# Performance work log

Hardware: AMD Instinct MI355X
Metric: run time of the kernel (lower is better)

Reference implementation:

```python
import jax, jax.numpy as jnp
import numpy as np

TEMP = 5.0      # torch_kmeans SoftKMeans default temperature
N_ITERS = 25    # fixed iteration count (tolerance-based stop removed for jit)
EPS = 1e-9


def _soft_kmeans(x, l, key):
    # x: (r, q, d) -> labels (r, q) int32, centers (r, l, d)
    r, q, d = x.shape
    keys = jax.random.split(key, r)
    # random-point init (one permutation per batch, first l points)
    idx = jax.vmap(lambda k: jax.random.permutation(k, q)[:l])(keys)  # (r, l)
    centers = jnp.take_along_axis(x, idx[:, :, None], axis=1)         # (r, l, d)
    x_sq = jnp.sum(x * x, axis=-1)                                    # (r, q)

    def dist_to(centers):
        # squared euclidean distance (r, q, l)
        return (x_sq[:, :, None]
                - 2.0 * jnp.einsum('rqd,rld->rql', x, centers)
                + jnp.sum(centers * centers, axis=-1)[:, None, :])

    def step(centers, _):
        w = jax.nn.softmax(-TEMP * dist_to(centers), axis=-1)         # (r, q, l)
        denom = jnp.sum(w, axis=1)[:, :, None] + EPS                  # (r, l, 1)
        centers = jnp.einsum('rql,rqd->rld', w, x) / denom
        return centers, None

    centers, _ = jax.lax.scan(step, centers, None, length=N_ITERS)
    labels = jnp.argmin(dist_to(centers), axis=-1)                    # (r, q)
    return labels, centers


def setup_inputs() -> dict:
    key = jax.random.key(0)
    x = jax.random.normal(key, (8, 2048, 1024), dtype=jnp.float32)
    return {"x": x, "q": 4096, "r": 8, "l": 256}


def reference(x, q, r, l):
    B, T, F = x.shape
    # B*T*F must equal r*q*d; mirrors x.view(B,-1).view(B,q,-1).view(r,q,-1)
    xr = x.reshape(r, q, -1)
    labels, centers = _soft_kmeans(xr, l, jax.random.key(42))
    # gather centroid per point: rec[b, i, :] = centers[b, labels[b, i], :]
    rec = jnp.take_along_axis(centers, labels[:, :, None], axis=1)    # (r, q, d)
    return rec.reshape(B, T, F)
```

## Files before the change

kernel.cpp:

```cpp
#include <hip/hip_runtime.h>
#include <stdint.h>

#define RB 8
#define QN 4096
#define DN 512
#define LN 256
#define NITERS 25

typedef double f64x4 __attribute__((ext_vector_type(4)));

__device__ __forceinline__ void tf2x32(uint32_t k0, uint32_t k1,
                                       uint32_t x0, uint32_t x1,
                                       uint32_t& y0, uint32_t& y1) {
  uint32_t ks2 = k0 ^ k1 ^ 0x1BD11BDAu;
#define TFR(r) { x0 += x1; x1 = (x1 << (r)) | (x1 >> (32 - (r))); x1 ^= x0; }
  x0 += k0; x1 += k1;
  TFR(13) TFR(15) TFR(26) TFR(6)   x0 += k1;  x1 += ks2 + 1u;
  TFR(17) TFR(29) TFR(16) TFR(24)  x0 += ks2; x1 += k0 + 2u;
  TFR(13) TFR(15) TFR(26) TFR(6)   x0 += k0;  x1 += k1 + 3u;
  TFR(17) TFR(29) TFR(16) TFR(24)  x0 += k1;  x1 += ks2 + 4u;
  TFR(13) TFR(15) TFR(26) TFR(6)   x0 += ks2; x1 += k0 + 5u;
#undef TFR
  y0 = x0; y1 = x1;
}

__global__ __launch_bounds__(1024) void k_init(const float* __restrict__ x,
                                               float* __restrict__ centers) {
  __shared__ unsigned long long comp[QN];
  __shared__ unsigned short perm[QN];
  __shared__ unsigned short ptmp[QN];
  const int b = blockIdx.x, t = threadIdx.x;

  uint32_t kb0, kb1;
  tf2x32(0u, 42u, 0u, (uint32_t)b, kb0, kb1);

  for (int i = t; i < QN; i += 1024) perm[i] = (unsigned short)i;
  __syncthreads();

  for (int round = 0; round < 2; ++round) {
    uint32_t nk0, nk1, sk0, sk1;
    tf2x32(kb0, kb1, 0u, 0u, nk0, nk1);
    tf2x32(kb0, kb1, 0u, 1u, sk0, sk1);
    kb0 = nk0; kb1 = nk1;
    for (int i = t; i < QN; i += 1024) {
      uint32_t y0, y1;
      tf2x32(sk0, sk1, 0u, (uint32_t)i, y0, y1);
      uint32_t bits = y0 ^ y1;
      comp[i] = ((unsigned long long)bits << 32) | (unsigned)i;
    }
    __syncthreads();
    for (int k = 2; k <= QN; k <<= 1) {
      for (int j = k >> 1; j > 0; j >>= 1) {
        for (int i = t; i < QN; i += 1024) {
          int ixj = i ^ j;
          if (ixj > i) {
            unsigned long long vi = comp[i], vj = comp[ixj];
            bool up = ((i & k) == 0);
            bool sw = up ? (vi > vj) : (vi < vj);
            if (sw) { comp[i] = vj; comp[ixj] = vi; }
          }
        }
        __syncthreads();
      }
    }
    for (int i = t; i < QN; i += 1024) ptmp[i] = perm[(unsigned)(comp[i] & 0xFFFFu)];
    __syncthreads();
    for (int i = t; i < QN; i += 1024) perm[i] = ptmp[i];
    __syncthreads();
  }

  const float4* xb = (const float4*)(x + (size_t)b * QN * DN);
  float4* cb = (float4*)(centers + (size_t)b * LN * DN);
  for (int e = t; e < LN * (DN / 4); e += 1024) {
    int row = e >> 7;
    int c = e & 127;
    cb[(size_t)row * 128 + c] = xb[(size_t)perm[row] * 128 + c];
  }
}

__global__ __launch_bounds__(256) void k_rowsq_d(const float* __restrict__ a,
                                                 double* __restrict__ o, int nrows) {
  int w = (blockIdx.x * 256 + threadIdx.x) >> 6;
  int lane = threadIdx.x & 63;
  if (w >= nrows) return;
  const float* row = a + (size_t)w * DN;
  double s = 0.0;
  for (int i = lane; i < DN; i += 64) { double v = (double)row[i]; s = fma(v, v, s); }
#pragma unroll
  for (int off = 32; off; off >>= 1) s += __shfl_down(s, off);
  if (lane == 0) o[w] = s;
}

__global__ __launch_bounds__(64) void k_probe(int* __restrict__ flag) {
  __shared__ double xT[16][17];
  __shared__ double cT[16][17];
  const int t = threadIdx.x;
  for (int i = t; i < 256; i += 64) {
    int r = i >> 4, d = i & 15;
    xT[d][r] = (double)(r * 5 + d * 3 + 1);
    cT[d][r] = (double)(r * 2 + d * 7 + 2);
  }
  __syncthreads();
  const int kg = t >> 4, li = t & 15;
  f64x4 acc = {0.0, 0.0, 0.0, 0.0};
#pragma unroll
  for (int kk = 0; kk < 4; kk++) {
    double a  = xT[kk * 4 + kg][li];
    double bv = cT[kk * 4 + kg][li];
    acc = __builtin_amdgcn_mfma_f64_16x16x4f64(a, bv, acc, 0, 0, 0);
  }
  bool ok1 = true, ok2 = true;
#pragma unroll
  for (int d = 0; d < 4; d++) {
    int q1 = kg * 4 + d;
    int q2 = kg + 4 * d;
    double ref1 = 0.0, ref2 = 0.0;
    for (int dd = 0; dd < 16; dd++) {
      ref1 += xT[dd][q1] * cT[dd][li];
      ref2 += xT[dd][q2] * cT[dd][li];
    }
    ok1 = ok1 && (acc[d] == ref1);
    ok2 = ok2 && (acc[d] == ref2);
  }
  unsigned long long v1 = __ballot(ok1);
  unsigned long long v2 = __ballot(ok2);
  if (t == 0) *flag = (v1 == ~0ull) ? 1 : ((v2 == ~0ull) ? 2 : 0);
}

#define QT 64
#define XPD 68
#define CPD 260
#define DK 16
#define XLD 82
#define CLDf 260
__device__ __forceinline__ int grow(int q) { return q + ((q >> 3) << 1); }

#define ARENA_D 5888

__global__ __launch_bounds__(256, 2) void k_assign(const float* __restrict__ x,
                                                   const float* __restrict__ centers,
                                                   const double* __restrict__ csqd,
                                                   float* __restrict__ W,
                                                   const int* __restrict__ flag) {
  __shared__ double arena[ARENA_D];
  const int mode = *flag;
  const int b = blockIdx.y, q0 = blockIdx.x * QT, t = threadIdx.x;
  const float* xb = x + ((size_t)b * QN + q0) * DN;
  const float* cb = centers + (size_t)b * LN * DN;
  const int xrow = t >> 2, xc4 = t & 3;

  if (mode != 0) {
    double (*xT)[XPD]  = (double(*)[XPD])arena;
    double (*cT)[CPD]  = (double(*)[CPD])(arena + 16 * XPD);
    double (*redm)[5]  = (double(*)[5])(arena + 16 * XPD + 16 * CPD);
    double (*reds)[5]  = (double(*)[5])(arena + 16 * XPD + 16 * CPD + 320);
    const int w = t >> 6, lane = t & 63;
    const int kg = lane >> 4, li = lane & 15;

    f64x4 acc[4][4];
#pragma unroll
    for (int i = 0; i < 4; i++)
#pragma unroll
      for (int j = 0; j < 4; j++) acc[i][j] = (f64x4){0.0, 0.0, 0.0, 0.0};

    float4 gx, gc[4];
    gx = *(const float4*)(xb + (size_t)xrow * DN + xc4 * 4);
#pragma unroll
    for (int i = 0; i < 4; i++) {
      int f = t + 256 * i; int row = f >> 2, c4 = f & 3;
      gc[i] = *(const float4*)(cb + (size_t)row * DN + c4 * 4);
    }

    for (int d0 = 0; d0 < DN; d0 += 16) {
      xT[xc4 * 4 + 0][xrow] = (double)gx.x;
      xT[xc4 * 4 + 1][xrow] = (double)gx.y;
      xT[xc4 * 4 + 2][xrow] = (double)gx.z;
      xT[xc4 * 4 + 3][xrow] = (double)gx.w;
#pragma unroll
      for (int i = 0; i < 4; i++) {
        int f = t + 256 * i; int row = f >> 2, c4 = f & 3;
        cT[c4 * 4 + 0][row] = (double)gc[i].x;
        cT[c4 * 4 + 1][row] = (double)gc[i].y;
        cT[c4 * 4 + 2][row] = (double)gc[i].z;
        cT[c4 * 4 + 3][row] = (double)gc[i].w;
      }
      __syncthreads();
      if (d0 + 16 < DN) {
        gx = *(const float4*)(xb + (size_t)xrow * DN + (d0 + 16) + xc4 * 4);
#pragma unroll
        for (int i = 0; i < 4; i++) {
          int f = t + 256 * i; int row = f >> 2, c4 = f & 3;
          gc[i] = *(const float4*)(cb + (size_t)row * DN + (d0 + 16) + c4 * 4);
        }
      }
#pragma unroll
      for (int kk = 0; kk < 4; kk++) {
        double a[4], bf[4];
#pragma unroll
        for (int qt = 0; qt < 4; qt++) a[qt] = xT[kk * 4 + kg][qt * 16 + li];
#pragma unroll
        for (int lt = 0; lt < 4; lt++) bf[lt] = cT[kk * 4 + kg][w * 64 + lt * 16 + li];
#pragma unroll
        for (int qt = 0; qt < 4; qt++)
#pragma unroll
          for (int lt = 0; lt < 4; lt++)
            acc[qt][lt] = __builtin_amdgcn_mfma_f64_16x16x4f64(a[qt], bf[lt], acc[qt][lt], 0, 0, 0);
      }
      __syncthreads();
    }

    double csqv[4];
#pragma unroll
    for (int lt = 0; lt < 4; lt++) csqv[lt] = csqd[b * LN + w * 64 + lt * 16 + li];

    double rm[4][4];
#pragma unroll
    for (int qt = 0; qt < 4; qt++)
#pragma unroll
      for (int d = 0; d < 4; d++) {
        double m = -1e300;
#pragma unroll
        for (int lt = 0; lt < 4; lt++) {
          double lg = -5.0 * (csqv[lt] - 2.0 * acc[qt][lt][d]);
          acc[qt][lt][d] = lg;
          m = fmax(m, lg);
        }
        rm[qt][d] = m;
      }
#pragma unroll
    for (int off = 1; off < 16; off <<= 1)
#pragma unroll
      for (int qt = 0; qt < 4; qt++)
#pragma unroll
        for (int d = 0; d < 4; d++) rm[qt][d] = fmax(rm[qt][d], __shfl_xor(rm[qt][d], off, 64));
    if (li == 0) {
#pragma unroll
      for (int qt = 0; qt < 4; qt++)
#pragma unroll
        for (int d = 0; d < 4; d++) {
          int qr = qt * 16 + ((mode == 1) ? (kg * 4 + d) : (kg + 4 * d));
          redm[qr][w] = rm[qt][d];
        }
    }
    __syncthreads();
#pragma unroll
    for (int qt = 0; qt < 4; qt++)
#pragma unroll
      for (int d = 0; d < 4; d++) {
        int qr = qt * 16 + ((mode == 1) ? (kg * 4 + d) : (kg + 4 * d));
        rm[qt][d] = fmax(fmax(redm[qr][0], redm[qr][1]), fmax(redm[qr][2], redm[qr][3]));
      }
    double sv[4][4];
#pragma unroll
    for (int qt = 0; qt < 4; qt++)
#pragma unroll
      for (int d = 0; d < 4; d++) {
        double s = 0.0;
#pragma unroll
        for (int lt = 0; lt < 4; lt++) {
          double e = exp(acc[qt][lt][d] - rm[qt][d]);
          acc[qt][lt][d] = e;
          s += e;
        }
        sv[qt][d] = s;
      }
#pragma unroll
    for (int off = 1; off < 16; off <<= 1)
#pragma unroll
      for (int qt = 0; qt < 4; qt++)
#pragma unroll
        for (int d = 0; d < 4; d++) sv[qt][d] += __shfl_xor(sv[qt][d], off, 64);
    if (li == 0) {
#pragma unroll
      for (int qt = 0; qt < 4; qt++)
#pragma unroll
        for (int d = 0; d < 4; d++) {
          int qr = qt * 16 + ((mode == 1) ? (kg * 4 + d) : (kg + 4 * d));
          reds[qr][w] = sv[qt][d];
        }
    }
    __syncthreads();
#pragma unroll
    for (int qt = 0; qt < 4; qt++)
#pragma unroll
      for (int d = 0; d < 4; d++) {
        int qr = qt * 16 + ((mode == 1) ? (kg * 4 + d) : (kg + 4 * d));
        double tot = reds[qr][0] + reds[qr][1] + reds[qr][2] + reds[qr][3];
        double inv = 1.0 / tot;
        float* wr = W + ((size_t)b * QN + q0 + qr) * LN + w * 64 + li;
#pragma unroll
        for (int lt = 0; lt < 4; lt++)
          wr[lt * 16] = (float)(acc[qt][lt][d] * inv);
      }
  } else {
    double (*xsD)[XLD]  = (double(*)[XLD])arena;
    float  (*csF)[CLDf] = (float(*)[CLDf])(arena + 16 * XLD);
    double (*red)[33]   = (double(*)[33])(arena + 16 * XLD + (16 * CLDf) / 2);
    const int rg = t & 7, cg = t >> 3;
    double acc[8][8];
#pragma unroll
    for (int i = 0; i < 8; i++)
#pragma unroll
      for (int j = 0; j < 8; j++) acc[i][j] = 0.0;

    const int xg = grow(xrow);
    float4 gx, gc[4];
    gx = *(const float4*)(xb + (size_t)xrow * DN + xc4 * 4);
#pragma unroll
    for (int i = 0; i < 4; i++) {
      int f = t + 256 * i; int row = f >> 2, c4 = f & 3;
      gc[i] = *(const float4*)(cb + (size_t)row * DN + c4 * 4);
    }

    for (int d0 = 0; d0 < DN; d0 += DK) {
      xsD[xc4 * 4 + 0][xg] = (double)gx.x; xsD[xc4 * 4 + 1][xg] = (double)gx.y;
      xsD[xc4 * 4 + 2][xg] = (double)gx.z; xsD[xc4 * 4 + 3][xg] = (double)gx.w;
#pragma unroll
      for (int i = 0; i < 4; i++) {
        int f = t + 256 * i; int row = f >> 2, c4 = f & 3;
        csF[c4 * 4 + 0][row] = gc[i].x; csF[c4 * 4 + 1][row] = gc[i].y;
        csF[c4 * 4 + 2][row] = gc[i].z; csF[c4 * 4 + 3][row] = gc[i].w;
      }
      __syncthreads();
      if (d0 + DK < DN) {
        gx = *(const float4*)(xb + (size_t)xrow * DN + (d0 + DK) + xc4 * 4);
#pragma unroll
        for (int i = 0; i < 4; i++) {
          int f = t + 256 * i; int row = f >> 2, c4 = f & 3;
          gc[i] = *(const float4*)(cb + (size_t)row * DN + (d0 + DK) + c4 * 4);
        }
      }
      double xva[8]; float4 ca0, ca1;
#pragma unroll
      for (int j = 0; j < 8; j++) xva[j] = xsD[0][rg * 10 + j];
      ca0 = *(const float4*)&csF[0][cg * 8];
      ca1 = *(const float4*)&csF[0][cg * 8 + 4];
#pragma unroll
      for (int k = 0; k < DK; k++) {
        double xvb[8]; float4 cb0, cb1;
        if (k + 1 < DK) {
#pragma unroll
          for (int j = 0; j < 8; j++) xvb[j] = xsD[k + 1][rg * 10 + j];
          cb0 = *(const float4*)&csF[k + 1][cg * 8];
          cb1 = *(const float4*)&csF[k + 1][cg * 8 + 4];
        }
        double cv[8] = {(double)ca0.x, (double)ca0.y, (double)ca0.z, (double)ca0.w,
                        (double)ca1.x, (double)ca1.y, (double)ca1.z, (double)ca1.w};
#pragma unroll
        for (int i = 0; i < 8; i++)
#pragma unroll
          for (int j = 0; j < 8; j++)
            acc[i][j] = fma(xva[i], cv[j], acc[i][j]);
        if (k + 1 < DK) {
#pragma unroll
          for (int j = 0; j < 8; j++) xva[j] = xvb[j];
          ca0 = cb0; ca1 = cb1;
        }
      }
      __syncthreads();
    }

    double csqv[8];
#pragma unroll
    for (int j = 0; j < 8; j++) csqv[j] = csqd[b * LN + cg * 8 + j];

    double lmax[8];
#pragma unroll
    for (int i = 0; i < 8; i++) {
      double m = -1e300;
#pragma unroll
      for (int j = 0; j < 8; j++) {
        double lg = -5.0 * (csqv[j] - 2.0 * acc[i][j]);
        acc[i][j] = lg;
        m = fmax(m, lg);
      }
      lmax[i] = m;
    }
#pragma unroll
    for (int i = 0; i < 8; i++) red[rg * 8 + i][cg] = lmax[i];
    __syncthreads();
    double rmax[8];
#pragma unroll
    for (int i = 0; i < 8; i++) {
      double m = -1e300;
      for (int c = 0; c < 32; c++) m = fmax(m, red[rg * 8 + i][c]);
      rmax[i] = m;
    }
    __syncthreads();
#pragma unroll
    for (int i = 0; i < 8; i++) {
      double s = 0.0;
#pragma unroll
      for (int j = 0; j < 8; j++) {
        double e = exp(acc[i][j] - rmax[i]);
        acc[i][j] = e;
        s += e;
      }
      red[rg * 8 + i][cg] = s;
    }
    __syncthreads();
#pragma unroll
    for (int i = 0; i < 8; i++) {
      double s = 0.0;
      for (int c = 0; c < 32; c++) s += red[rg * 8 + i][c];
      float* wrow = W + ((size_t)b * QN + q0 + rg * 8 + i) * LN + cg * 8;
      float4 v0 = make_float4((float)(acc[i][0] / s), (float)(acc[i][1] / s),
                              (float)(acc[i][2] / s), (float)(acc[i][3] / s));
      float4 v1 = make_float4((float)(acc[i][4] / s), (float)(acc[i][5] / s),
                              (float)(acc[i][6] / s), (float)(acc[i][7] / s));
      *(float4*)wrow = v0;
      *(float4*)(wrow + 4) = v1;
    }
  }
}

#define NCH 8
#define CHQ (QN / NCH)
#define UKQ 16

__global__ __launch_bounds__(256, 3) void k_update_split(
    const float* __restrict__ W, const float* __restrict__ x,
    float* __restrict__ P, float* __restrict__ dsum) {
  __shared__ float wT[UKQ][132];
  __shared__ float xT[UKQ][132];
  const int b = blockIdx.z;
  const int s = blockIdx.y;
  const int lt = (blockIdx.x >> 2) * 128;
  const int dt = (blockIdx.x & 3) * 128;
  const int t = threadIdx.x;
  const int tr = t >> 4, tc = t & 15;
  float acc[8][8];
#pragma unroll
  for (int i = 0; i < 8; i++)
#pragma unroll
    for (int j = 0; j < 8; j++) acc[i][j] = 0.f;
  float dsm[8] = {0, 0, 0, 0, 0, 0, 0, 0};

  const float* Wb = W + ((size_t)b * QN + (size_t)s * CHQ) * LN + lt;
  const float* xb = x + ((size_t)b * QN + (size_t)s * CHQ) * DN + dt;

  float4 gw[2], gx2[2];
#pragma unroll
  for (int i = 0; i < 2; i++) {
    int f = t + 256 * i; int row = f >> 5, c = f & 31;
    gw[i]  = *(const float4*)(Wb + (size_t)row * LN + c * 4);
    gx2[i] = *(const float4*)(xb + (size_t)row * DN + c * 4);
  }

  for (int k0 = 0; k0 < CHQ; k0 += UKQ) {
#pragma unroll
    for (int i = 0; i < 2; i++) {
      int f = t + 256 * i; int row = f >> 5, c = f & 31;
      *(float4*)&wT[row][c * 4] = gw[i];
      *(float4*)&xT[row][c * 4] = gx2[i];
    }
    __syncthreads();
    if (k0 + UKQ < CHQ) {
#pragma unroll
      for (int i = 0; i < 2; i++) {
        int f = t + 256 * i; int row = f >> 5, c = f & 31;
        gw[i]  = *(const float4*)(Wb + (size_t)(k0 + UKQ + row) * LN + c * 4);
        gx2[i] = *(const float4*)(xb + (size_t)(k0 + UKQ + row) * DN + c * 4);
      }
    }
#pragma unroll
    for (int k = 0; k < UKQ; k++) {
      float4 w0 = *(const float4*)&wT[k][tr * 4];
      float4 w1 = *(const float4*)&wT[k][64 + tr * 4];
      float4 x0 = *(const float4*)&xT[k][tc * 4];
      float4 x1 = *(const float4*)&xT[k][64 + tc * 4];
      float wf[8] = {w0.x, w0.y, w0.z, w0.w, w1.x, w1.y, w1.z, w1.w};
      float xf[8] = {x0.x, x0.y, x0.z, x0.w, x1.x, x1.y, x1.z, x1.w};
#pragma unroll
      for (int i = 0; i < 8; i++) {
        dsm[i] += wf[i];
#pragma unroll
        for (int j = 0; j < 8; j++) acc[i][j] = fmaf(wf[i], xf[j], acc[i][j]);
      }
    }
    __syncthreads();
  }

#pragma unroll
  for (int i = 0; i < 8; i++) {
    int l = lt + ((i < 4) ? (tr * 4 + i) : (64 + tr * 4 + i - 4));
    float* prow = P + (((size_t)s * RB + b) * LN + l) * DN + dt;
    *(float4*)(prow + tc * 4)      = make_float4(acc[i][0], acc[i][1], acc[i][2], acc[i][3]);
    *(float4*)(prow + 64 + tc * 4) = make_float4(acc[i][4], acc[i][5], acc[i][6], acc[i][7]);
    if (tc == 0) dsum[((size_t)s * RB + b) * LN + l] = dsm[i];
  }
}

__global__ __launch_bounds__(128) void k_reduce(const float* __restrict__ P,
                                                const float* __restrict__ dsum,
                                                float* __restrict__ cnew,
                                                double* __restrict__ csqd) {
  const int row = blockIdx.x;
  const int b = row >> 8, l = row & 255;
  const int t = threadIdx.x;
  float dn = 0.f;
#pragma unroll
  for (int s = 0; s < NCH; s++) dn += dsum[((size_t)s * RB + b) * LN + l];
  float den = dn + 1e-9f;
  float4 v = make_float4(0.f, 0.f, 0.f, 0.f);
#pragma unroll
  for (int s = 0; s < NCH; s++) {
    float4 p = *(const float4*)(P + (((size_t)s * RB + b) * LN + l) * DN + t * 4);
    v.x += p.x; v.y += p.y; v.z += p.z; v.w += p.w;
  }
  float4 o = make_float4(v.x / den, v.y / den, v.z / den, v.w / den);
  *(float4*)(cnew + ((size_t)b * LN + l) * DN + t * 4) = o;
  double sq = (double)o.x * o.x + (double)o.y * o.y +
              (double)o.z * o.z + (double)o.w * o.w;
#pragma unroll
  for (int off = 32; off; off >>= 1) sq += __shfl_down(sq, off);
  __shared__ double sred[2];
  if ((t & 63) == 0) sred[t >> 6] = sq;
  __syncthreads();
  if (t == 0) csqd[row] = sred[0] + sred[1];
}

#define LT 64
#define DT 64
#define KQ 32
__global__ __launch_bounds__(256) void k_update_mono(const float* __restrict__ W,
                                                     const float* __restrict__ x,
                                                     float* __restrict__ cnew) {
  __shared__ float wT[KQ][LT + 4];
  __shared__ float xT[KQ][DT + 4];
  const int b = blockIdx.z;
  const int l0 = blockIdx.x * LT;
  const int d0 = blockIdx.y * DT;
  const int t = threadIdx.x;
  const int rg = t & 15;
  const int cg = t >> 4;
  float acc[4][4];
#pragma unroll
  for (int i = 0; i < 4; i++)
#pragma unroll
    for (int j = 0; j < 4; j++) acc[i][j] = 0.f;
  float dsm[4] = {0.f, 0.f, 0.f, 0.f};
  const float* Wb = W + (size_t)b * QN * LN;
  const float* xb = x + (size_t)b * QN * DN;
  for (int k0 = 0; k0 < QN; k0 += KQ) {
#pragma unroll
    for (int i = 0; i < 2; i++) {
      int f = t + 256 * i;
      int row = f >> 4, c4 = f & 15;
      *(float4*)&wT[row][c4 * 4] = *(const float4*)(Wb + (size_t)(k0 + row) * LN + l0 + c4 * 4);
    }
#pragma unroll
    for (int i = 0; i < 2; i++) {
      int f = t + 256 * i;
      int row = f >> 4, c4 = f & 15;
      *(float4*)&xT[row][c4 * 4] = *(const float4*)(xb + (size_t)(k0 + row) * DN + d0 + c4 * 4);
    }
    __syncthreads();
#pragma unroll
    for (int k = 0; k < KQ; k++) {
      float wf[4], xf[4];
      *(float4*)wf = *(const float4*)&wT[k][rg * 4];
      *(float4*)xf = *(const float4*)&xT[k][cg * 4];
#pragma unroll
      for (int i = 0; i < 4; i++) {
        dsm[i] += wf[i];
#pragma unroll
        for (int j = 0; j < 4; j++) acc[i][j] = fmaf(wf[i], xf[j], acc[i][j]);
      }
    }
    __syncthreads();
  }
#pragma unroll
  for (int i = 0; i < 4; i++) {
    float den = dsm[i] + 1e-9f;
    *(float4*)(cnew + ((size_t)b * LN + l0 + rg * 4 + i) * DN + d0 + cg * 4) =
        make_float4(acc[i][0] / den, acc[i][1] / den, acc[i][2] / den, acc[i][3] / den);
  }
}

__global__ __launch_bounds__(256, 2) void k_final(const float* __restrict__ x,
                                                  const float* __restrict__ centers,
                                                  const double* __restrict__ csqd,
                                                  float* __restrict__ out) {
  __shared__ double xsD[DK][XLD];
  __shared__ float  csF[DK][CLDf];
  __shared__ double redv[QT][33];
  __shared__ unsigned short redi[QT][33];
  __shared__ unsigned short labels[QT];
  const int b = blockIdx.y, q0 = blockIdx.x * QT, t = threadIdx.x;
  const int rg = t & 7, cg = t >> 3;
  double acc[8][8];
#pragma unroll
  for (int i = 0; i < 8; i++)
#pragma unroll
    for (int j = 0; j < 8; j++) acc[i][j] = 0.0;

  const float* xb = x + ((size_t)b * QN + q0) * DN;
  const float* cb = centers + (size_t)b * LN * DN;
  const int xrow = t >> 2, xc4 = t & 3;
  const int xg = grow(xrow);

  float4 gx, gc[4];
  gx = *(const float4*)(xb + (size_t)xrow * DN + xc4 * 4);
#pragma unroll
  for (int i = 0; i < 4; i++) {
    int f = t + 256 * i; int row = f >> 2, c4 = f & 3;
    gc[i] = *(const float4*)(cb + (size_t)row * DN + c4 * 4);
  }

  for (int d0 = 0; d0 < DN; d0 += DK) {
    xsD[xc4 * 4 + 0][xg] = (double)gx.x; xsD[xc4 * 4 + 1][xg] = (double)gx.y;
    xsD[xc4 * 4 + 2][xg] = (double)gx.z; xsD[xc4 * 4 + 3][xg] = (double)gx.w;
#pragma unroll
    for (int i = 0; i < 4; i++) {
      int f = t + 256 * i; int row = f >> 2, c4 = f & 3;
      csF[c4 * 4 + 0][row] = gc[i].x; csF[c4 * 4 + 1][row] = gc[i].y;
      csF[c4 * 4 + 2][row] = gc[i].z; csF[c4 * 4 + 3][row] = gc[i].w;
    }
    __syncthreads();
    if (d0 + DK < DN) {
      gx = *(const float4*)(xb + (size_t)xrow * DN + (d0 + DK) + xc4 * 4);
#pragma unroll
      for (int i = 0; i < 4; i++) {
        int f = t + 256 * i; int row = f >> 2, c4 = f & 3;
        gc[i] = *(const float4*)(cb + (size_t)row * DN + (d0 + DK) + c4 * 4);
      }
    }
    double xva[8]; float4 ca0, ca1;
#pragma unroll
    for (int j = 0; j < 8; j++) xva[j] = xsD[0][rg * 10 + j];
    ca0 = *(const float4*)&csF[0][cg * 8];
    ca1 = *(const float4*)&csF[0][cg * 8 + 4];
#pragma unroll
    for (int k = 0; k < DK; k++) {
      double xvb[8]; float4 cb0, cb1;
      if (k + 1 < DK) {
#pragma unroll
        for (int j = 0; j < 8; j++) xvb[j] = xsD[k + 1][rg * 10 + j];
        cb0 = *(const float4*)&csF[k + 1][cg * 8];
        cb1 = *(const float4*)&csF[k + 1][cg * 8 + 4];
      }
      double cv[8] = {(double)ca0.x, (double)ca0.y, (double)ca0.z, (double)ca0.w,
                      (double)ca1.x, (double)ca1.y, (double)ca1.z, (double)ca1.w};
#pragma unroll
      for (int i = 0; i < 8; i++)
#pragma unroll
        for (int j = 0; j < 8; j++)
          acc[i][j] = fma(xva[i], cv[j], acc[i][j]);
      if (k + 1 < DK) {
#pragma unroll
        for (int j = 0; j < 8; j++) xva[j] = xvb[j];
        ca0 = cb0; ca1 = cb1;
      }
    }
    __syncthreads();
  }

  double csqv[8];
#pragma unroll
  for (int j = 0; j < 8; j++) csqv[j] = csqd[b * LN + cg * 8 + j];

  double bv[8]; int bi[8];
#pragma unroll
  for (int i = 0; i < 8; i++) {
    bv[i] = 1e300; bi[i] = 0;
#pragma unroll
    for (int j = 0; j < 8; j++) {
      double dd = csqv[j] - 2.0 * acc[i][j];
      if (dd < bv[i]) { bv[i] = dd; bi[i] = cg * 8 + j; }
    }
  }
#pragma unroll
  for (int i = 0; i < 8; i++) {
    redv[rg * 8 + i][cg] = bv[i];
    redi[rg * 8 + i][cg] = (unsigned short)bi[i];
  }
  __syncthreads();
  if (t < QT) {
    double best = 1e300; int bidx = 0;
    for (int c = 0; c < 32; c++) {
      double v = redv[t][c];
      int id = redi[t][c];
      if (v < best || (v == best && id < bidx)) { best = v; bidx = id; }
    }
    labels[t] = (unsigned short)bidx;
  }
  __syncthreads();
  const float4* cb4 = (const float4*)(centers + (size_t)b * LN * DN);
  float4* ob = (float4*)(out + ((size_t)b * QN + q0) * DN);
  for (int e = t; e < QT * (DN / 4); e += 256) {
    int row = e >> 7, c = e & 127;
    ob[(size_t)row * 128 + c] = cb4[(size_t)labels[row] * 128 + c];
  }
}

extern "C" void kernel_launch(void* const* d_in, const int* in_sizes, int n_in,
                              void* d_out, int out_size, void* d_ws, size_t ws_size,
                              hipStream_t stream) {
  const float* x = (const float*)d_in[0];
  float* out = (float*)d_out;

  const size_t szC    = (size_t)RB * LN * DN * sizeof(float);
  const size_t szCsqD = (size_t)RB * LN * sizeof(double);
  const size_t szDsum = (size_t)NCH * RB * LN * sizeof(float);
  const size_t szFlag = 256;
  const size_t szW    = (size_t)RB * QN * LN * sizeof(float);

  char* p = (char*)d_ws;
  float*  cA   = (float*)p;  p += szC;
  float*  cB   = (float*)p;  p += szC;
  double* csqd = (double*)p; p += szCsqD;
  float*  dsum = (float*)p;  p += szDsum;
  int*    flag = (int*)p;    p += szFlag;
  const bool bigws = ws_size >= 2 * szC + szCsqD + szDsum + szFlag + szW;
  float* W = bigws ? (float*)p : (float*)d_out;
  float* P = (float*)d_out;

  k_probe<<<1, 64, 0, stream>>>(flag);
  k_init<<<RB, 1024, 0, stream>>>(x, cA);
  k_rowsq_d<<<(RB * LN) / 4, 256, 0, stream>>>(cA, csqd, RB * LN);

  float* cur = cA;
  float* nxt = cB;
  for (int it = 0; it < NITERS; ++it) {
    k_assign<<<dim3(QN / QT, RB), 256, 0, stream>>>(x, cur, csqd, W, flag);
    if (bigws) {
      k_update_split<<<dim3(8, NCH, RB), 256, 0, stream>>>(W, x, P, dsum);
      k_reduce<<<RB * LN, 128, 0, stream>>>(P, dsum, nxt, csqd);
    } else {
      k_update_mono<<<dim3(LN / LT, DN / DT, RB), 256, 0, stream>>>(W, x, nxt);
      k_rowsq_d<<<(RB * LN) / 4, 256, 0, stream>>>(nxt, csqd, RB * LN);
    }
    float* tmp = cur; cur = nxt; nxt = tmp;
  }
  k_final<<<dim3(QN / QT, RB), 256, 0, stream>>>(x, cur, csqd, out);
}
```

Before: 8.011 ms.

## Use f64 MFMA in final assignment kernel, prefetch fragments, pad LDS

Ports the final labeling kernel from a scalar FP64 FMA outer product to the f64 MFMA path already used by k_assign. It reduces the argmin with wave shuffles and a small cross-wave LDS reduction. The old scalar path is kept as a fallback chosen by the probe flag. In both kernels it also double-buffers the LDS fragment loads across the k-steps and changes the LDS row padding to odd strides to cut bank conflicts. The final kernel runs only once, so most of the gain would come from the assign tweaks, which run every iteration; the extra live registers could hurt occupancy.

New measurement: 7.589 ms, median of 2. -5.3%, faster.

```diff
diff --git a/kernel.cpp b/kernel.cpp
--- a/kernel.cpp
+++ b/kernel.cpp
@@ -128,14 +128,14 @@
 }
 
 #define QT 64
-#define XPD 68
-#define CPD 260
+#define XPD 69
+#define CPD 261
 #define DK 16
 #define XLD 82
 #define CLDf 260
 __device__ __forceinline__ int grow(int q) { return q + ((q >> 3) << 1); }
 
-#define ARENA_D 5888
+#define ARENA_D 5920
 
 __global__ __launch_bounds__(256, 2) void k_assign(const float* __restrict__ x,
                                                    const float* __restrict__ centers,
@@ -193,18 +193,31 @@
           gc[i] = *(const float4*)(cb + (size_t)row * DN + (d0 + 16) + c4 * 4);
         }
       }
+      double a0[4], b0[4];
+#pragma unroll
+      for (int qt = 0; qt < 4; qt++) a0[qt] = xT[kg][qt * 16 + li];
+#pragma unroll
+      for (int lt = 0; lt < 4; lt++) b0[lt] = cT[kg][w * 64 + lt * 16 + li];
 #pragma unroll
       for (int kk = 0; kk < 4; kk++) {
-        double a[4], bf[4];
-#pragma unroll
-        for (int qt = 0; qt < 4; qt++) a[qt] = xT[kk * 4 + kg][qt * 16 + li];
-#pragma unroll
-        for (int lt = 0; lt < 4; lt++) bf[lt] = cT[kk * 4 + kg][w * 64 + lt * 16 + li];
+        double a1[4], b1[4];
+        if (kk + 1 < 4) {
+#pragma unroll
+          for (int qt = 0; qt < 4; qt++) a1[qt] = xT[(kk + 1) * 4 + kg][qt * 16 + li];
+#pragma unroll
+          for (int lt = 0; lt < 4; lt++) b1[lt] = cT[(kk + 1) * 4 + kg][w * 64 + lt * 16 + li];
+        }
 #pragma unroll
         for (int qt = 0; qt < 4; qt++)
 #pragma unroll
           for (int lt = 0; lt < 4; lt++)
-            acc[qt][lt] = __builtin_amdgcn_mfma_f64_16x16x4f64(a[qt], bf[lt], acc[qt][lt], 0, 0, 0);
+            acc[qt][lt] = __builtin_amdgcn_mfma_f64_16x16x4f64(a0[qt], b0[lt], acc[qt][lt], 0, 0, 0);
+        if (kk + 1 < 4) {
+#pragma unroll
+          for (int qt = 0; qt < 4; qt++) a0[qt] = a1[qt];
+#pragma unroll
+          for (int lt = 0; lt < 4; lt++) b0[lt] = b1[lt];
+        }
       }
       __syncthreads();
     }
@@ -578,119 +591,256 @@
   }
 }
 
+#define ARENA_F 6048
 __global__ __launch_bounds__(256, 2) void k_final(const float* __restrict__ x,
                                                   const float* __restrict__ centers,
                                                   const double* __restrict__ csqd,
-                                                  float* __restrict__ out) {
-  __shared__ double xsD[DK][XLD];
-  __shared__ float  csF[DK][CLDf];
-  __shared__ double redv[QT][33];
-  __shared__ unsigned short redi[QT][33];
-  __shared__ unsigned short labels[QT];
+                                                  float* __restrict__ out,
+                                                  const int* __restrict__ flag) {
+  __shared__ double arena[ARENA_F];
+  const int mode = *flag;
   const int b = blockIdx.y, q0 = blockIdx.x * QT, t = threadIdx.x;
-  const int rg = t & 7, cg = t >> 3;
-  double acc[8][8];
-#pragma unroll
-  for (int i = 0; i < 8; i++)
-#pragma unroll
-    for (int j = 0; j < 8; j++) acc[i][j] = 0.0;
-
   const float* xb = x + ((size_t)b * QN + q0) * DN;
   const float* cb = centers + (size_t)b * LN * DN;
   const int xrow = t >> 2, xc4 = t & 3;
-  const int xg = grow(xrow);
-
-  float4 gx, gc[4];
-  gx = *(const float4*)(xb + (size_t)xrow * DN + xc4 * 4);
-#pragma unroll
-  for (int i = 0; i < 4; i++) {
-    int f = t + 256 * i; int row = f >> 2, c4 = f & 3;
-    gc[i] = *(const float4*)(cb + (size_t)row * DN + c4 * 4);
-  }
-
-  for (int d0 = 0; d0 < DN; d0 += DK) {
-    xsD[xc4 * 4 + 0][xg] = (double)gx.x; xsD[xc4 * 4 + 1][xg] = (double)gx.y;
-    xsD[xc4 * 4 + 2][xg] = (double)gx.z; xsD[xc4 * 4 + 3][xg] = (double)gx.w;
+
+  if (mode != 0) {
+    double (*xT)[XPD] = (double(*)[XPD])arena;
+    double (*cT)[CPD] = (double(*)[CPD])(arena + 16 * XPD);
+    double (*redv)[5] = (double(*)[5])(arena + 16 * XPD + 16 * CPD);
+    int*    redi      = (int*)(arena + 16 * XPD + 16 * CPD + 320);
+    unsigned short* labels = (unsigned short*)(arena + 16 * XPD + 16 * CPD + 480);
+    const int w = t >> 6, lane = t & 63;
+    const int kg = lane >> 4, li = lane & 15;
+
+    f64x4 acc[4][4];
+#pragma unroll
+    for (int i = 0; i < 4; i++)
+#pragma unroll
+      for (int j = 0; j < 4; j++) acc[i][j] = (f64x4){0.0, 0.0, 0.0, 0.0};
+
+    float4 gx, gc[4];
+    gx = *(const float4*)(xb + (size_t)xrow * DN + xc4 * 4);
 #pragma unroll
     for (int i = 0; i < 4; i++) {
       int f = t + 256 * i; int row = f >> 2, c4 = f & 3;
-      csF[c4 * 4 + 0][row] = gc[i].x; csF[c4 * 4 + 1][row] = gc[i].y;
-      csF[c4 * 4 + 2][row] = gc[i].z; csF[c4 * 4 + 3][row] = gc[i].w;
-    }
-    __syncthreads();
-    if (d0 + DK < DN) {
-      gx = *(const float4*)(xb + (size_t)xrow * DN + (d0 + DK) + xc4 * 4);
+      gc[i] = *(const float4*)(cb + (size_t)row * DN + c4 * 4);
+    }
+
+    for (int d0 = 0; d0 < DN; d0 += 16) {
+      xT[xc4 * 4 + 0][xrow] = (double)gx.x;
+      xT[xc4 * 4 + 1][xrow] = (double)gx.y;
+      xT[xc4 * 4 + 2][xrow] = (double)gx.z;
+      xT[xc4 * 4 + 3][xrow] = (double)gx.w;
 #pragma unroll
       for (int i = 0; i < 4; i++) {
         int f = t + 256 * i; int row = f >> 2, c4 = f & 3;
-        gc[i] = *(const float4*)(cb + (size_t)row * DN + (d0 + DK) + c4 * 4);
-      }
-    }
-    double xva[8]; float4 ca0, ca1;
-#pragma unroll
-    for (int j = 0; j < 8; j++) xva[j] = xsD[0][rg * 10 + j];
-    ca0 = *(const float4*)&csF[0][cg * 8];
-    ca1 = *(const float4*)&csF[0][cg * 8 + 4];
-#pragma unroll
-    for (int k = 0; k < DK; k++) {
-      double xvb[8]; float4 cb0, cb1;
-      if (k + 1 < DK) {
-#pragma unroll
-        for (int j = 0; j < 8; j++) xvb[j] = xsD[k + 1][rg * 10 + j];
-        cb0 = *(const float4*)&csF[k + 1][cg * 8];
-        cb1 = *(const float4*)&csF[k + 1][cg * 8 + 4];
-      }
-      double cv[8] = {(double)ca0.x, (double)ca0.y, (double)ca0.z, (double)ca0.w,
-                      (double)ca1.x, (double)ca1.y, (double)ca1.z, (double)ca1.w};
-#pragma unroll
-      for (int i = 0; i < 8; i++)
-#pragma unroll
-        for (int j = 0; j < 8; j++)
-          acc[i][j] = fma(xva[i], cv[j], acc[i][j]);
-      if (k + 1 < DK) {
-#pragma unroll
-        for (int j = 0; j < 8; j++) xva[j] = xvb[j];
-        ca0 = cb0; ca1 = cb1;
-      }
-    }
-    __syncthreads();
-  }
-
-  double csqv[8];
-#pragma unroll
-  for (int j = 0; j < 8; j++) csqv[j] = csqd[b * LN + cg * 8 + j];
-
-  double bv[8]; int bi[8];
-#pragma unroll
-  for (int i = 0; i < 8; i++) {
-    bv[i] = 1e300; bi[i] = 0;
-#pragma unroll
-    for (int j = 0; j < 8; j++) {
-      double dd = csqv[j] - 2.0 * acc[i][j];
-      if (dd < bv[i]) { bv[i] = dd; bi[i] = cg * 8 + j; }
-    }
-  }
-#pragma unroll
-  for (int i = 0; i < 8; i++) {
-    redv[rg * 8 + i][cg] = bv[i];
-    redi[rg * 8 + i][cg] = (unsigned short)bi[i];
-  }
-  __syncthreads();
-  if (t < QT) {
-    double best = 1e300; int bidx = 0;
-    for (int c = 0; c < 32; c++) {
-      double v = redv[t][c];
-      int id = redi[t][c];
-      if (v < best || (v == best && id < bidx)) { best = v; bidx = id; }
-    }
-    labels[t] = (unsigned short)bidx;
-  }
-  __syncthreads();
-  const float4* cb4 = (const float4*)(centers + (size_t)b * LN * DN);
-  float4* ob = (float4*)(out + ((size_t)b * QN + q0) * DN);
-  for (int e = t; e < QT * (DN / 4); e += 256) {
-    int row = e >> 7, c = e & 127;
-    ob[(size_t)row * 128 + c] = cb4[(size_t)labels[row] * 128 + c];
+        cT[c4 * 4 + 0][row] = (double)gc[i].x;
+        cT[c4 * 4 + 1][row] = (double)gc[i].y;
+        cT[c4 * 4 + 2][row] = (double)gc[i].z;
+        cT[c4 * 4 + 3][row] = (double)gc[i].w;
+      }
+      __syncthreads();
+      if (d0 + 16 < DN) {
+        gx = *(const float4*)(xb + (size_t)xrow * DN + (d0 + 16) + xc4 * 4);
+#pragma unroll
+        for (int i = 0; i < 4; i++) {
+          int f = t + 256 * i; int row = f >> 2, c4 = f & 3;
+          gc[i] = *(const float4*)(cb + (size_t)row * DN + (d0 + 16) + c4 * 4);
+        }
+      }
+      double a0[4], b0[4];
+#pragma unroll
+      for (int qt = 0; qt < 4; qt++) a0[qt] = xT[kg][qt * 16 + li];
+#pragma unroll
+      for (int lt = 0; lt < 4; lt++) b0[lt] = cT[kg][w * 64 + lt * 16 + li];
+#pragma unroll
+      for (int kk = 0; kk < 4; kk++) {
+        double a1[4], b1[4];
+        if (kk + 1 < 4) {
+#pragma unroll
+          for (int qt = 0; qt < 4; qt++) a1[qt] = xT[(kk + 1) * 4 + kg][qt * 16 + li];
+#pragma unroll
+          for (int lt = 0; lt < 4; lt++) b1[lt] = cT[(kk + 1) * 4 + kg][w * 64 + lt * 16 + li];
+        }
+#pragma unroll
+        for (int qt = 0; qt < 4; qt++)
+#pragma unroll
+          for (int lt = 0; lt < 4; lt++)
+            acc[qt][lt] = __builtin_amdgcn_mfma_f64_16x16x4f64(a0[qt], b0[lt], acc[qt][lt], 0, 0, 0);
+        if (kk + 1 < 4) {
+#pragma unroll
+          for (int qt = 0; qt < 4; qt++) a0[qt] = a1[qt];
+#pragma unroll
+          for (int lt = 0; lt < 4; lt++) b0[lt] = b1[lt];
+        }
+      }
+      __syncthreads();
+    }
+
+    double csqv[4];
+#pragma unroll
+    for (int lt = 0; lt < 4; lt++) csqv[lt] = csqd[b * LN + w * 64 + lt * 16 + li];
+
+    double bv[4][4]; int bi[4][4];
+#pragma unroll
+    for (int qt = 0; qt < 4; qt++)
+#pragma unroll
+      for (int d = 0; d < 4; d++) {
+        double best = 1e300; int bidx = 0;
+#pragma unroll
+        for (int lt = 0; lt < 4; lt++) {
+          double dd = csqv[lt] - 2.0 * acc[qt][lt][d];
+          int l = w * 64 + lt * 16 + li;
+          if (dd < best) { best = dd; bidx = l; }
+        }
+        bv[qt][d] = best; bi[qt][d] = bidx;
+      }
+#pragma unroll
+    for (int off = 1; off < 16; off <<= 1)
+#pragma unroll
+      for (int qt = 0; qt < 4; qt++)
+#pragma unroll
+        for (int d = 0; d < 4; d++) {
+          double ov = __shfl_xor(bv[qt][d], off, 64);
+          int oi = __shfl_xor(bi[qt][d], off, 64);
+          if (ov < bv[qt][d] || (ov == bv[qt][d] && oi < bi[qt][d])) {
+            bv[qt][d] = ov; bi[qt][d] = oi;
+          }
+        }
+    if (li == 0) {
+#pragma unroll
+      for (int qt = 0; qt < 4; qt++)
+#pragma unroll
+        for (int d = 0; d < 4; d++) {
+          int qr = qt * 16 + ((mode == 1) ? (kg * 4 + d) : (kg + 4 * d));
+          redv[qr][w] = bv[qt][d];
+          redi[qr * 5 + w] = bi[qt][d];
+        }
+    }
+    __syncthreads();
+    if (t < QT) {
+      double best = redv[t][0]; int bidx = redi[t * 5 + 0];
+#pragma unroll
+      for (int ww = 1; ww < 4; ww++) {
+        double v = redv[t][ww]; int id = redi[t * 5 + ww];
+        if (v < best || (v == best && id < bidx)) { best = v; bidx = id; }
+      }
+      labels[t] = (unsigned short)bidx;
+    }
+    __syncthreads();
+    const float4* cb4 = (const float4*)(centers + (size_t)b * LN * DN);
+    float4* ob = (float4*)(out + ((size_t)b * QN + q0) * DN);
+    for (int e = t; e < QT * (DN / 4); e += 256) {
+      int row = e >> 7, c = e & 127;
+      ob[(size_t)row * 128 + c] = cb4[(size_t)labels[row] * 128 + c];
+    }
+  } else {
+    double (*xsD)[XLD]  = (double(*)[XLD])arena;
+    float  (*csF)[CLDf] = (float(*)[CLDf])(arena + 16 * XLD);
+    double (*redv)[33]  = (double(*)[33])(arena + 3392);
+    unsigned short* redi = (unsigned short*)(arena + 5504);
+    unsigned short* labels = (unsigned short*)(arena + 6032);
+    const int rg = t & 7, cg = t >> 3;
+    double acc[8][8];
+#pragma unroll
+    for (int i = 0; i < 8; i++)
+#pragma unroll
+      for (int j = 0; j < 8; j++) acc[i][j] = 0.0;
+
+    const int xg = grow(xrow);
+    float4 gx, gc[4];
+    gx = *(const float4*)(xb + (size_t)xrow * DN + xc4 * 4);
+#pragma unroll
+    for (int i = 0; i < 4; i++) {
+      int f = t + 256 * i; int row = f >> 2, c4 = f & 3;
+      gc[i] = *(const float4*)(cb + (size_t)row * DN + c4 * 4);
+    }
+
+    for (int d0 = 0; d0 < DN; d0 += DK) {
+      xsD[xc4 * 4 + 0][xg] = (double)gx.x; xsD[xc4 * 4 + 1][xg] = (double)gx.y;
+      xsD[xc4 * 4 + 2][xg] = (double)gx.z; xsD[xc4 * 4 + 3][xg] = (double)gx.w;
+#pragma unroll
+      for (int i = 0; i < 4; i++) {
+        int f = t + 256 * i; int row = f >> 2, c4 = f & 3;
+        csF[c4 * 4 + 0][row] = gc[i].x; csF[c4 * 4 + 1][row] = gc[i].y;
+        csF[c4 * 4 + 2][row] = gc[i].z; csF[c4 * 4 + 3][row] = gc[i].w;
+      }
+      __syncthreads();
+      if (d0 + DK < DN) {
+        gx = *(const float4*)(xb + (size_t)xrow * DN + (d0 + DK) + xc4 * 4);
+#pragma unroll
+        for (int i = 0; i < 4; i++) {
+          int f = t + 256 * i; int row = f >> 2, c4 = f & 3;
+          gc[i] = *(const float4*)(cb + (size_t)row * DN + (d0 + DK) + c4 * 4);
+        }
+      }
+      double xva[8]; float4 ca0, ca1;
+#pragma unroll
+      for (int j = 0; j < 8; j++) xva[j] = xsD[0][rg * 10 + j];
+      ca0 = *(const float4*)&csF[0][cg * 8];
+      ca1 = *(const float4*)&csF[0][cg * 8 + 4];
+#pragma unroll
+      for (int k = 0; k < DK; k++) {
+        double xvb[8]; float4 cb0, cb1;
+        if (k + 1 < DK) {
+#pragma unroll
+          for (int j = 0; j < 8; j++) xvb[j] = xsD[k + 1][rg * 10 + j];
+          cb0 = *(const float4*)&csF[k + 1][cg * 8];
+          cb1 = *(const float4*)&csF[k + 1][cg * 8 + 4];
+        }
+        double cv[8] = {(double)ca0.x, (double)ca0.y, (double)ca0.z, (double)ca0.w,
+                        (double)ca1.x, (double)ca1.y, (double)ca1.z, (double)ca1.w};
+#pragma unroll
+        for (int i = 0; i < 8; i++)
+#pragma unroll
+          for (int j = 0; j < 8; j++)
+            acc[i][j] = fma(xva[i], cv[j], acc[i][j]);
+        if (k + 1 < DK) {
+#pragma unroll
+          for (int j = 0; j < 8; j++) xva[j] = xvb[j];
+          ca0 = cb0; ca1 = cb1;
+        }
+      }
+      __syncthreads();
+    }
+
+    double csqv[8];
+#pragma unroll
+    for (int j = 0; j < 8; j++) csqv[j] = csqd[b * LN + cg * 8 + j];
+
+    double bv[8]; int bi[8];
+#pragma unroll
+    for (int i = 0; i < 8; i++) {
+      bv[i] = 1e300; bi[i] = 0;
+#pragma unroll
+      for (int j = 0; j < 8; j++) {
+        double dd = csqv[j] - 2.0 * acc[i][j];
+        if (dd < bv[i]) { bv[i] = dd; bi[i] = cg * 8 + j; }
+      }
+    }
+#pragma unroll
+    for (int i = 0; i < 8; i++) {
+      redv[rg * 8 + i][cg] = bv[i];
+      redi[(rg * 8 + i) * 33 + cg] = (unsigned short)bi[i];
+    }
+    __syncthreads();
+    if (t < QT) {
+      double best = 1e300; int bidx = 0;
+      for (int c = 0; c < 32; c++) {
+        double v = redv[t][c];
+        int id = redi[t * 33 + c];
+        if (v < best || (v == best && id < bidx)) { best = v; bidx = id; }
+      }
+      labels[t] = (unsigned short)bidx;
+    }
+    __syncthreads();
+    const float4* cb4 = (const float4*)(centers + (size_t)b * LN * DN);
+    float4* ob = (float4*)(out + ((size_t)b * QN + q0) * DN);
+    for (int e = t; e < QT * (DN / 4); e += 256) {
+      int row = e >> 7, c = e & 127;
+      ob[(size_t)row * 128 + c] = cb4[(size_t)labels[row] * 128 + c];
+    }
   }
 }
 
@@ -733,5 +883,5 @@
     }
     float* tmp = cur; cur = nxt; nxt = tmp;
   }
-  k_final<<<dim3(QN / QT, RB), 256, 0, stream>>>(x, cur, csqd, out);
-}
+  k_final<<<dim3(QN / QT, RB), 256, 0, stream>>>(x, cur, csqd, out, flag);
+}
```
